# Kernel optimization log

Measured on AMD Instinct MI355X. Metric: run time of the kernel, lower is better.

Reference implementation:

```python
import jax, jax.numpy as jnp
import numpy as np


def log_g(x):
    # log of g(x) = x + 0.5 for x>=0, sigmoid(x) for x<0
    return jnp.where(x >= 0, jnp.log(jax.nn.relu(x) + 0.5), -jax.nn.softplus(-x))


def setup_inputs() -> dict:
    key = jax.random.key(0)
    k1, k2 = jax.random.split(key)
    B, S, D = 4, 4096, 1024
    x = jax.random.normal(k1, (B, S, D), dtype=jnp.float32)
    # nn.Linear(dim, 2*dim, bias=False) weight: [2*dim, dim], scaled like kaiming-uniform-ish
    W = jax.random.normal(k2, (2 * D, D), dtype=jnp.float32) * (1.0 / np.sqrt(D))
    return {"x": x, "W": W}


def reference(x, W):
    # x: [B, S, D], W: [2D, D] -> hidden, gate: [B, S, D]
    hg = jnp.einsum("bsd,ed->bse", x, W)
    hidden, gate = jnp.split(hg, 2, axis=-1)

    log_coeffs = -jax.nn.softplus(gate)        # log(1 - z)
    log_z = -jax.nn.softplus(-gate)            # log(z)
    log_values = log_z + log_g(hidden)

    # Heinsen associative scan in log space along seq axis
    a_star = jnp.cumsum(log_coeffs, axis=1)
    log_h0_plus_b_star = jax.lax.cumlogsumexp(log_values - a_star, axis=1)
    log_h = a_star + log_h0_plus_b_star
    out = jnp.exp(log_h)                       # [B, S, D]
    # expansion_factor == 1.0 -> to_out is Identity
    return out
```

## Files before the change

kernel.cpp:

```cpp
#include <hip/hip_runtime.h>
#include <hip/hip_bf16.h>
#include <hip/hip_fp16.h>
#include <math.h>

#define B_  4
#define S_  4096
#define D_  1024
#define M_  (B_ * S_)
#define K_  D_
#define L_  32
#define NC_ (S_ / L_)
#define NKT 32

typedef __attribute__((ext_vector_type(8))) short          bf16x8;
typedef __attribute__((ext_vector_type(8))) unsigned short u16x8;
typedef __attribute__((ext_vector_type(4))) float          f32x4;

__device__ __forceinline__ unsigned short f2bf(float f) {
    union { __hip_bfloat16 h; unsigned short u; } cv;
    cv.h = __float2bfloat16(f);
    return cv.u;
}

__device__ __forceinline__ float fast_rcp(float x) {
#if __has_builtin(__builtin_amdgcn_rcpf)
    return __builtin_amdgcn_rcpf(x);
#else
    return 1.0f / x;
#endif
}

__device__ __forceinline__ void stage16(const unsigned short* src, char* dst) {
    __builtin_amdgcn_global_load_lds(
        (const __attribute__((address_space(1))) unsigned int*)src,
        (__attribute__((address_space(3))) unsigned int*)dst, 16, 0, 0);
}

__global__ __launch_bounds__(256) void to_bf16_both(
    const float* __restrict__ x, const float* __restrict__ W,
    unsigned short* __restrict__ xb, unsigned short* __restrict__ Wb,
    int n8x, int n8w)
{
    int i = blockIdx.x * 256 + threadIdx.x;
    const float* src;
    unsigned short* dst;
    int j;
    if (i < n8x) { src = x; dst = xb; j = i; }
    else {
        j = i - n8x;
        if (j >= n8w) return;
        src = W; dst = Wb;
    }
    const float4* p = (const float4*)src + (size_t)j * 2;
    float4 a = p[0], b = p[1];
    u16x8 o;
    o[0] = f2bf(a.x); o[1] = f2bf(a.y); o[2] = f2bf(a.z); o[3] = f2bf(a.w);
    o[4] = f2bf(b.x); o[5] = f2bf(b.y); o[6] = f2bf(b.z); o[7] = f2bf(b.w);
    *(u16x8*)(dst + (size_t)j * 8) = o;
}

__global__ __launch_bounds__(256, 2) void gemm_pointwise(
    const unsigned short* __restrict__ xb, const unsigned short* __restrict__ Wb,
    __half2* __restrict__ cvb, float2* __restrict__ CVagg)
{
    __shared__ char lds[73728];

    const int th   = threadIdx.x;
    const int lane = th & 63;
    const int wave = th >> 6;
    const int wm = wave >> 1;
    const int wn = wave & 1;

    const int wg  = blockIdx.x;
    const int swz = (wg & 7) * 128 + (wg >> 3);
    const int m0 = (swz >> 3) * 128;
    const int d0 = (swz & 7) * 128;

    f32x4 acc[4][8];
#pragma unroll
    for (int i = 0; i < 4; ++i)
#pragma unroll
        for (int j = 0; j < 8; ++j)
            acc[i][j] = (f32x4){0.f, 0.f, 0.f, 0.f};

    const int srow = th >> 2;
    const int scol = (((th & 3) ^ ((th >> 3) & 3)) * 8);
    const unsigned short* srcA  = xb + (size_t)(m0 + srow)      * K_ + scol;
    const unsigned short* srcBh = Wb + (size_t)(d0 + srow)      * K_ + scol;
    const unsigned short* srcBg = Wb + (size_t)(D_ + d0 + srow) * K_ + scol;
    char* const wuo = lds + wave * 1024;

    const int lr = lane & 15;
    const int lq = lane >> 4;
    const int lkb = ((lq ^ ((lr >> 1) & 3)) * 16);
    const int aoffb = (wm * 64 + lr) * 64 + lkb;
    const int boffh = 8192 + (wn * 64 + lr) * 64 + lkb;
    const int boffg = boffh + 8192;

    bf16x8 Af[4], Bf[8];

#define BAR()  asm volatile("s_barrier" ::: "memory")
#define LGK0() asm volatile("s_waitcnt lgkmcnt(0)" ::: "memory")
#define VMW6() asm volatile("s_waitcnt vmcnt(6)" ::: "memory")
#define VMW0() asm volatile("s_waitcnt vmcnt(0)" ::: "memory")

#define STAGE_AH(tt, q) do { const int ko_ = (tt) * 32;                   \
    stage16(srcA  + ko_,            (q));                                 \
    stage16(srcA  + 64 * K_ + ko_,  (q) + 4096);                          \
    stage16(srcBh + ko_,            (q) + 8192);                          \
    stage16(srcBh + 64 * K_ + ko_,  (q) + 12288); } while (0)
#define STAGE_G(tt, q) do { const int ko_ = (tt) * 32;                    \
    stage16(srcBg + ko_,            (q) + 16384);                         \
    stage16(srcBg + 64 * K_ + ko_,  (q) + 20480); } while (0)

#define TILEBODY(T, P0, Q2, PRE, WAITOP) do {                             \
    _Pragma("unroll")                                                     \
    for (int i_ = 0; i_ < 4; ++i_)                                        \
        Af[i_] = *(const bf16x8*)((P0) + aoffb + i_ * 1024);              \
    _Pragma("unroll")                                                     \
    for (int j_ = 0; j_ < 4; ++j_)                                        \
        Bf[j_] = *(const bf16x8*)((P0) + boffh + j_ * 1024);              \
    if (PRE) { STAGE_AH((T) + 2, (Q2)); }                                 \
    BAR(); LGK0();                                                        \
    __builtin_amdgcn_s_setprio(1);                                        \
    _Pragma("unroll")                                                     \
    for (int i_ = 0; i_ < 4; ++i_)                                        \
        _Pragma("unroll")                                                 \
        for (int j_ = 0; j_ < 4; ++j_)                                    \
            acc[i_][j_] = __builtin_amdgcn_mfma_f32_16x16x32_bf16(        \
                Af[i_], Bf[j_], acc[i_][j_], 0, 0, 0);                    \
    __builtin_amdgcn_s_setprio(0);                                        \
    BAR();                                                                \
    _Pragma("unroll")                                                     \
    for (int j_ = 0; j_ < 4; ++j_)                                        \
        Bf[4 + j_] = *(const bf16x8*)((P0) + boffg + j_ * 1024);          \
    if (PRE) { STAGE_G((T) + 2, (Q2)); }                                  \
    BAR(); LGK0();                                                        \
    __builtin_amdgcn_s_setprio(1);                                        \
    _Pragma("unroll")                                                     \
    for (int i_ = 0; i_ < 4; ++i_)                                        \
        _Pragma("unroll")                                                 \
        for (int j_ = 0; j_ < 4; ++j_)                                    \
            acc[i_][4 + j_] = __builtin_amdgcn_mfma_f32_16x16x32_bf16(    \
                Af[i_], Bf[4 + j_], acc[i_][4 + j_], 0, 0, 0);            \
    __builtin_amdgcn_s_setprio(0);                                        \
    WAITOP;                                                               \
    BAR();                                                                \
  } while (0)

    const char* p0 = lds;
    const char* p1 = lds + 24576;
    const char* p2 = lds + 49152;
    char* q0 = wuo;
    char* q1 = wuo + 24576;
    char* q2 = wuo + 49152;

    STAGE_AH(0, q0); STAGE_G(0, q0);
    STAGE_AH(1, q1); STAGE_G(1, q1);
    VMW6();
    BAR();

#pragma unroll 1
    for (int t = 0; t < NKT - 2; ++t) {
        TILEBODY(t, p0, q2, 1, VMW6());
        const char* tp = p0; p0 = p1; p1 = p2; p2 = tp;
        char* tq = q0; q0 = q1; q1 = q2; q2 = tq;
    }
    TILEBODY(NKT - 2, p0, q2, 0, VMW0());
    { const char* tp = p0; p0 = p1; p1 = p2; p2 = tp; }
    TILEBODY(NKT - 1, p0, q2, 0, (void)0);

#undef TILEBODY
#undef STAGE_AH
#undef STAGE_G
#undef BAR
#undef LGK0
#undef VMW6
#undef VMW0

#pragma unroll
    for (int mp = 0; mp < 2; ++mp) {
        float C16[2][4], V16[2][4];
#pragma unroll
        for (int hf = 0; hf < 2; ++hf) {
            const int mi = mp * 2 + hf;
#pragma unroll
            for (int nj = 0; nj < 4; ++nj) {
                float C4 = 1.0f, V4 = 0.0f;
                const int d = d0 + wn * 64 + nj * 16 + lr;
#pragma unroll
                for (int r = 0; r < 4; ++r) {
                    int m = m0 + wm * 64 + mi * 16 + lq * 4 + r;
                    float h = acc[mi][nj][r];
                    float g = acc[mi][nj + 4][r];
                    float eg  = __expf(g);
                    float c   = fast_rcp(1.0f + eg);
                    float z   = eg * c;
                    float enh = __expf(-h);
                    float sh  = fast_rcp(1.0f + enh);
                    float gh  = (h >= 0.0f) ? (h + 0.5f) : sh;
                    float v   = z * gh;
                    cvb[(size_t)m * D_ + d] = __floats2half2_rn(c, v);
                    V4 = fmaf(c, V4, v);
                    C4 *= c;
                }
                float Ca = __shfl_xor(C4, 16), Va = __shfl_xor(V4, 16);
                float Clo = (lq & 1) ? Ca : C4, Vlo = (lq & 1) ? Va : V4;
                float Chi = (lq & 1) ? C4 : Ca, Vhi = (lq & 1) ? V4 : Va;
                float C2 = Clo * Chi, V2 = fmaf(Chi, Vlo, Vhi);
                float Cb = __shfl_xor(C2, 32), Vb = __shfl_xor(V2, 32);
                float Cl2 = (lq & 2) ? Cb : C2, Vl2 = (lq & 2) ? Vb : V2;
                float Ch2 = (lq & 2) ? C2 : Cb, Vh2 = (lq & 2) ? V2 : Vb;
                C16[hf][nj] = Cl2 * Ch2;
                V16[hf][nj] = fmaf(Ch2, Vl2, Vh2);
            }
        }
        if (lq == 0) {
            const int chunkg = (m0 + wm * 64 + mp * 32) >> 5;
#pragma unroll
            for (int nj = 0; nj < 4; ++nj) {
                float C32 = C16[0][nj] * C16[1][nj];
                float V32 = fmaf(C16[1][nj], V16[0][nj], V16[1][nj]);
                const int d = d0 + wn * 64 + nj * 16 + lr;
                float2 st; st.x = C32; st.y = V32;
                CVagg[(size_t)chunkg * D_ + d] = st;
            }
        }
    }
}

__global__ __launch_bounds__(256) void chunk_scan(
    const float2* __restrict__ CVagg, float* __restrict__ P)
{
    const int d = blockIdx.x * 256 + threadIdx.x;
    const int b = blockIdx.z;
    float h = 0.0f;
    for (int c = 0; c < NC_; ++c) {
        size_t o = ((size_t)b * NC_ + c) * D_ + d;
        P[o] = h;
        float2 cv = CVagg[o];
        h = fmaf(cv.x, h, cv.y);
    }
}

__global__ __launch_bounds__(256) void chunk_apply(
    const unsigned int* __restrict__ cvw, const float* __restrict__ P,
    float* __restrict__ out)
{
    const int d = (blockIdx.x * 256 + threadIdx.x) * 2;
    const int c = blockIdx.y;
    const int b = blockIdx.z;
    size_t base = ((size_t)(b * S_ + c * L_)) * D_ + d;
    float2 h2 = *(const float2*)(P + ((size_t)b * NC_ + c) * D_ + d);
    float h0 = h2.x, h1 = h2.y;
    for (int s = 0; s < L_; ++s) {
        uint2 u = *(const uint2*)(cvw + base + (size_t)s * D_);
        float2 p0 = __half22float2(*(const __half2*)&u.x);
        float2 p1 = __half22float2(*(const __half2*)&u.y);
        h0 = fmaf(p0.x, h0, p0.y);
        h1 = fmaf(p1.x, h1, p1.y);
        float2 o2 = {h0, h1};
        *(float2*)(out + base + (size_t)s * D_) = o2;
    }
}

extern "C" void kernel_launch(void* const* d_in, const int* in_sizes, int n_in,
                              void* d_out, int out_size, void* d_ws, size_t ws_size,
                              hipStream_t stream) {
    const float* x = (const float*)d_in[0];
    const float* W = (const float*)d_in[1];
    float* out = (float*)d_out;

    float2* CVagg = (float2*)d_ws;
    float*  P     = (float*)(CVagg + (size_t)B_ * NC_ * D_);
    __half2* cvb  = (__half2*)(P + (size_t)B_ * NC_ * D_);
    unsigned short* xb = (unsigned short*)(cvb + (size_t)M_ * D_);
    unsigned short* Wb = xb + (size_t)M_ * K_;

    const int n8x = M_ * K_ / 8;
    const int n8w = 2 * D_ * K_ / 8;
    to_bf16_both<<<(n8x + n8w + 255) / 256, 256, 0, stream>>>(x, W, xb, Wb, n8x, n8w);

    gemm_pointwise<<<1024, 256, 0, stream>>>(xb, Wb, cvb, CVagg);

    dim3 g3(D_ / 256, 1, B_);
    chunk_scan<<<g3, 256, 0, stream>>>(CVagg, P);

    dim3 g2(D_ / 512, NC_, B_);
    chunk_apply<<<g2, 256, 0, stream>>>((const unsigned int*)cvb, P, out);
}
```

Before: 129.8 us.

## Enlarge GEMM tile to 256 rows with 8 waves and 32x32 MFMA

The fused GEMM+pointwise kernel moves from a 128x128 tile with 4 waves to a 256-row tile with 8 waves (512 threads), and switches from 16x16x32 to 32x32x16 bf16 MFMA. Each wave now owns 128 rows by 32 hidden/gate columns, so the epilogue's chunk reduction uses a single cross-half shuffle. The aim is more operand reuse per LDS load and fewer MFMA issues. The cost is more LDS (96KB) and larger accumulator register pressure, which may limit occupancy.

```diff
diff --git a/kernel.cpp b/kernel.cpp
--- a/kernel.cpp
+++ b/kernel.cpp
@@ -12,9 +12,9 @@
 #define NC_ (S_ / L_)
 #define NKT 32
 
-typedef __attribute__((ext_vector_type(8))) short          bf16x8;
-typedef __attribute__((ext_vector_type(8))) unsigned short u16x8;
-typedef __attribute__((ext_vector_type(4))) float          f32x4;
+typedef __attribute__((ext_vector_type(8)))  short          bf16x8;
+typedef __attribute__((ext_vector_type(8)))  unsigned short u16x8;
+typedef __attribute__((ext_vector_type(16))) float          f32x16;
 
 __device__ __forceinline__ unsigned short f2bf(float f) {
     union { __hip_bfloat16 h; unsigned short u; } cv;
@@ -59,110 +59,115 @@
     *(u16x8*)(dst + (size_t)j * 8) = o;
 }
 
-__global__ __launch_bounds__(256, 2) void gemm_pointwise(
+__global__ __launch_bounds__(512, 2) void gemm_pointwise(
     const unsigned short* __restrict__ xb, const unsigned short* __restrict__ Wb,
     __half2* __restrict__ cvb, float2* __restrict__ CVagg)
 {
-    __shared__ char lds[73728];
+    __shared__ char lds[98304];
 
     const int th   = threadIdx.x;
     const int lane = th & 63;
     const int wave = th >> 6;
-    const int wm = wave >> 1;
-    const int wn = wave & 1;
+    const int wm = wave >> 2;
+    const int wn = wave & 3;
 
     const int wg  = blockIdx.x;
-    const int swz = (wg & 7) * 128 + (wg >> 3);
-    const int m0 = (swz >> 3) * 128;
+    const int swz = (wg & 7) * 64 + (wg >> 3);
+    const int m0 = (swz >> 3) * 256;
     const int d0 = (swz & 7) * 128;
 
-    f32x4 acc[4][8];
+    f32x16 acch[4], accg[4];
 #pragma unroll
     for (int i = 0; i < 4; ++i)
 #pragma unroll
-        for (int j = 0; j < 8; ++j)
-            acc[i][j] = (f32x4){0.f, 0.f, 0.f, 0.f};
+        for (int r = 0; r < 16; ++r) { acch[i][r] = 0.0f; accg[i][r] = 0.0f; }
 
     const int srow = th >> 2;
     const int scol = (((th & 3) ^ ((th >> 3) & 3)) * 8);
-    const unsigned short* srcA  = xb + (size_t)(m0 + srow)      * K_ + scol;
-    const unsigned short* srcBh = Wb + (size_t)(d0 + srow)      * K_ + scol;
-    const unsigned short* srcBg = Wb + (size_t)(D_ + d0 + srow) * K_ + scol;
+    const unsigned short* srcA  = xb + (size_t)(m0 + srow)       * K_ + scol;
+    const unsigned short* srcA2 = xb + (size_t)(m0 + 128 + srow) * K_ + scol;
+    const unsigned short* srcBh = Wb + (size_t)(d0 + srow)       * K_ + scol;
+    const unsigned short* srcBg = Wb + (size_t)(D_ + d0 + srow)  * K_ + scol;
     char* const wuo = lds + wave * 1024;
 
-    const int lr = lane & 15;
-    const int lq = lane >> 4;
-    const int lkb = ((lq ^ ((lr >> 1) & 3)) * 16);
-    const int aoffb = (wm * 64 + lr) * 64 + lkb;
-    const int boffh = 8192 + (wn * 64 + lr) * 64 + lkb;
-    const int boffg = boffh + 8192;
-
-    bf16x8 Af[4], Bf[8];
+    const int r31 = lane & 31;
+    const int l5  = lane >> 5;
+    const int sx  = (r31 >> 1) & 3;
+    const int ko0 = (l5 ^ sx) * 16;
+    const int ko1 = ko0 ^ 32;
+    const int abase  = (wm * 128 + r31) * 64;
+    const int bbaseh = 16384 + (wn * 32 + r31) * 64;
+    const int bbaseg = bbaseh + 8192;
+
+    bf16x8 Af[4], Bh, Bg;
 
 #define BAR()  asm volatile("s_barrier" ::: "memory")
 #define LGK0() asm volatile("s_waitcnt lgkmcnt(0)" ::: "memory")
-#define VMW6() asm volatile("s_waitcnt vmcnt(6)" ::: "memory")
+#define VMW4() asm volatile("s_waitcnt vmcnt(4)" ::: "memory")
 #define VMW0() asm volatile("s_waitcnt vmcnt(0)" ::: "memory")
 
-#define STAGE_AH(tt, q) do { const int ko_ = (tt) * 32;                   \
-    stage16(srcA  + ko_,            (q));                                 \
-    stage16(srcA  + 64 * K_ + ko_,  (q) + 4096);                          \
-    stage16(srcBh + ko_,            (q) + 8192);                          \
-    stage16(srcBh + 64 * K_ + ko_,  (q) + 12288); } while (0)
-#define STAGE_G(tt, q) do { const int ko_ = (tt) * 32;                    \
-    stage16(srcBg + ko_,            (q) + 16384);                         \
-    stage16(srcBg + 64 * K_ + ko_,  (q) + 20480); } while (0)
+#define STAGE_A(tt, q) do { const int ko_ = (tt) * 32;                    \
+    stage16(srcA  + ko_, (q));                                            \
+    stage16(srcA2 + ko_, (q) + 8192); } while (0)
+#define STAGE_B(tt, q) do { const int ko_ = (tt) * 32;                    \
+    stage16(srcBh + ko_, (q) + 16384);                                    \
+    stage16(srcBg + ko_, (q) + 24576); } while (0)
 
 #define TILEBODY(T, P0, Q2, PRE, WAITOP) do {                             \
+                                                       \
     _Pragma("unroll")                                                     \
     for (int i_ = 0; i_ < 4; ++i_)                                        \
-        Af[i_] = *(const bf16x8*)((P0) + aoffb + i_ * 1024);              \
-    _Pragma("unroll")                                                     \
-    for (int j_ = 0; j_ < 4; ++j_)                                        \
-        Bf[j_] = *(const bf16x8*)((P0) + boffh + j_ * 1024);              \
-    if (PRE) { STAGE_AH((T) + 2, (Q2)); }                                 \
+        Af[i_] = *(const bf16x8*)((P0) + abase + i_ * 2048 + ko0);        \
+    Bh = *(const bf16x8*)((P0) + bbaseh + ko0);                           \
+    Bg = *(const bf16x8*)((P0) + bbaseg + ko0);                           \
+    if (PRE) { STAGE_A((T) + 2, (Q2)); }                                  \
     BAR(); LGK0();                                                        \
     __builtin_amdgcn_s_setprio(1);                                        \
     _Pragma("unroll")                                                     \
-    for (int i_ = 0; i_ < 4; ++i_)                                        \
-        _Pragma("unroll")                                                 \
-        for (int j_ = 0; j_ < 4; ++j_)                                    \
-            acc[i_][j_] = __builtin_amdgcn_mfma_f32_16x16x32_bf16(        \
-                Af[i_], Bf[j_], acc[i_][j_], 0, 0, 0);                    \
+    for (int i_ = 0; i_ < 4; ++i_) {                                      \
+        acch[i_] = __builtin_amdgcn_mfma_f32_32x32x16_bf16(               \
+            Af[i_], Bh, acch[i_], 0, 0, 0);                               \
+        accg[i_] = __builtin_amdgcn_mfma_f32_32x32x16_bf16(               \
+            Af[i_], Bg, accg[i_], 0, 0, 0);                               \
+    }                                                                     \
     __builtin_amdgcn_s_setprio(0);                                        \
     BAR();                                                                \
-    _Pragma("unroll")                                                     \
-    for (int j_ = 0; j_ < 4; ++j_)                                        \
-        Bf[4 + j_] = *(const bf16x8*)((P0) + boffg + j_ * 1024);          \
-    if (PRE) { STAGE_G((T) + 2, (Q2)); }                                  \
+                                                       \
+    _Pragma("unroll")                                                     \
+    for (int i_ = 0; i_ < 4; ++i_)                                        \
+        Af[i_] = *(const bf16x8*)((P0) + abase + i_ * 2048 + ko1);        \
+    Bh = *(const bf16x8*)((P0) + bbaseh + ko1);                           \
+    Bg = *(const bf16x8*)((P0) + bbaseg + ko1);                           \
+    if (PRE) { STAGE_B((T) + 2, (Q2)); }                                  \
     BAR(); LGK0();                                                        \
     __builtin_amdgcn_s_setprio(1);                                        \
     _Pragma("unroll")                                                     \
-    for (int i_ = 0; i_ < 4; ++i_)                                        \
-        _Pragma("unroll")                                                 \
-        for (int j_ = 0; j_ < 4; ++j_)                                    \
-            acc[i_][4 + j_] = __builtin_amdgcn_mfma_f32_16x16x32_bf16(    \
-                Af[i_], Bf[4 + j_], acc[i_][4 + j_], 0, 0, 0);            \
+    for (int i_ = 0; i_ < 4; ++i_) {                                      \
+        acch[i_] = __builtin_amdgcn_mfma_f32_32x32x16_bf16(               \
+            Af[i_], Bh, acch[i_], 0, 0, 0);                               \
+        accg[i_] = __builtin_amdgcn_mfma_f32_32x32x16_bf16(               \
+            Af[i_], Bg, accg[i_], 0, 0, 0);                               \
+    }                                                                     \
     __builtin_amdgcn_s_setprio(0);                                        \
     WAITOP;                                                               \
     BAR();                                                                \
   } while (0)
 
     const char* p0 = lds;
-    const char* p1 = lds + 24576;
-    const char* p2 = lds + 49152;
+    const char* p1 = lds + 32768;
+    const char* p2 = lds + 65536;
     char* q0 = wuo;
-    char* q1 = wuo + 24576;
-    char* q2 = wuo + 49152;
-
-    STAGE_AH(0, q0); STAGE_G(0, q0);
-    STAGE_AH(1, q1); STAGE_G(1, q1);
-    VMW6();
+    char* q1 = wuo + 32768;
+    char* q2 = wuo + 65536;
+
+    STAGE_A(0, q0); STAGE_B(0, q0);
+    STAGE_A(1, q1); STAGE_B(1, q1);
+    VMW4();
     BAR();
 
 #pragma unroll 1
     for (int t = 0; t < NKT - 2; ++t) {
-        TILEBODY(t, p0, q2, 1, VMW6());
+        TILEBODY(t, p0, q2, 1, VMW4());
         const char* tp = p0; p0 = p1; p1 = p2; p2 = tp;
         char* tq = q0; q0 = q1; q1 = q2; q2 = tq;
     }
@@ -171,60 +176,54 @@
     TILEBODY(NKT - 1, p0, q2, 0, (void)0);
 
 #undef TILEBODY
-#undef STAGE_AH
-#undef STAGE_G
+#undef STAGE_A
+#undef STAGE_B
 #undef BAR
 #undef LGK0
-#undef VMW6
+#undef VMW4
 #undef VMW0
 
-#pragma unroll
-    for (int mp = 0; mp < 2; ++mp) {
-        float C16[2][4], V16[2][4];
-#pragma unroll
-        for (int hf = 0; hf < 2; ++hf) {
-            const int mi = mp * 2 + hf;
-#pragma unroll
-            for (int nj = 0; nj < 4; ++nj) {
-                float C4 = 1.0f, V4 = 0.0f;
-                const int d = d0 + wn * 64 + nj * 16 + lr;
-#pragma unroll
-                for (int r = 0; r < 4; ++r) {
-                    int m = m0 + wm * 64 + mi * 16 + lq * 4 + r;
-                    float h = acc[mi][nj][r];
-                    float g = acc[mi][nj + 4][r];
-                    float eg  = __expf(g);
-                    float c   = fast_rcp(1.0f + eg);
-                    float z   = eg * c;
-                    float enh = __expf(-h);
-                    float sh  = fast_rcp(1.0f + enh);
-                    float gh  = (h >= 0.0f) ? (h + 0.5f) : sh;
-                    float v   = z * gh;
-                    cvb[(size_t)m * D_ + d] = __floats2half2_rn(c, v);
-                    V4 = fmaf(c, V4, v);
-                    C4 *= c;
-                }
-                float Ca = __shfl_xor(C4, 16), Va = __shfl_xor(V4, 16);
-                float Clo = (lq & 1) ? Ca : C4, Vlo = (lq & 1) ? Va : V4;
-                float Chi = (lq & 1) ? C4 : Ca, Vhi = (lq & 1) ? V4 : Va;
-                float C2 = Clo * Chi, V2 = fmaf(Chi, Vlo, Vhi);
-                float Cb = __shfl_xor(C2, 32), Vb = __shfl_xor(V2, 32);
-                float Cl2 = (lq & 2) ? Cb : C2, Vl2 = (lq & 2) ? Vb : V2;
-                float Ch2 = (lq & 2) ? C2 : Cb, Vh2 = (lq & 2) ? V2 : Vb;
-                C16[hf][nj] = Cl2 * Ch2;
-                V16[hf][nj] = fmaf(Ch2, Vl2, Vh2);
-            }
+    const int d = d0 + wn * 32 + r31;
+#pragma unroll
+    for (int mt = 0; mt < 4; ++mt) {
+        float C4[4], V4[4];
+#pragma unroll
+        for (int q = 0; q < 4; ++q) { C4[q] = 1.0f; V4[q] = 0.0f; }
+#pragma unroll
+        for (int reg = 0; reg < 16; ++reg) {
+            const int q = reg >> 2;
+            const int m = m0 + wm * 128 + mt * 32 + (reg & 3) + 8 * q + 4 * l5;
+            float h = acch[mt][reg];
+            float g = accg[mt][reg];
+            float eg  = __expf(g);
+            float c   = fast_rcp(1.0f + eg);
+            float z   = eg * c;
+            float enh = __expf(-h);
+            float sh  = fast_rcp(1.0f + enh);
+            float gh  = (h >= 0.0f) ? (h + 0.5f) : sh;
+            float v   = z * gh;
+            cvb[(size_t)m * D_ + d] = __floats2half2_rn(c, v);
+            V4[q] = fmaf(c, V4[q], v);
+            C4[q] *= c;
         }
-        if (lq == 0) {
-            const int chunkg = (m0 + wm * 64 + mp * 32) >> 5;
-#pragma unroll
-            for (int nj = 0; nj < 4; ++nj) {
-                float C32 = C16[0][nj] * C16[1][nj];
-                float V32 = fmaf(C16[1][nj], V16[0][nj], V16[1][nj]);
-                const int d = d0 + wn * 64 + nj * 16 + lr;
-                float2 st; st.x = C32; st.y = V32;
-                CVagg[(size_t)chunkg * D_ + d] = st;
-            }
+        float Cc = 1.0f, Vv = 0.0f;
+#pragma unroll
+        for (int q = 0; q < 4; ++q) {
+            float Cp = __shfl_xor(C4[q], 32);
+            float Vp = __shfl_xor(V4[q], 32);
+            float Clo = l5 ? Cp : C4[q];
+            float Vlo = l5 ? Vp : V4[q];
+            float Chi = l5 ? C4[q] : Cp;
+            float Vhi = l5 ? V4[q] : Vp;
+            float C8 = Chi * Clo;
+            float V8 = fmaf(Chi, Vlo, Vhi);
+            Vv = fmaf(C8, Vv, V8);
+            Cc = C8 * Cc;
+        }
+        if (l5 == 0) {
+            const int chunkg = (m0 + wm * 128 + mt * 32) >> 5;
+            float2 st; st.x = Cc; st.y = Vv;
+            CVagg[(size_t)chunkg * D_ + d] = st;
         }
     }
 }
@@ -281,7 +280,7 @@
     const int n8w = 2 * D_ * K_ / 8;
     to_bf16_both<<<(n8x + n8w + 255) / 256, 256, 0, stream>>>(x, W, xb, Wb, n8x, n8w);
 
-    gemm_pointwise<<<1024, 256, 0, stream>>>(xb, Wb, cvb, CVagg);
+    gemm_pointwise<<<512, 512, 0, stream>>>(xb, Wb, cvb, CVagg);
 
     dim3 g3(D_ / 256, 1, B_);
     chunk_scan<<<g3, 256, 0, stream>>>(CVagg, P);
```

Result: slower. 133.4 us (+2.7%).
